# Kernel optimization log

Hardware: AMD Instinct MI355X
Metric: run time of the kernel (lower is better)

Reference implementation:

```python
import jax, jax.numpy as jnp
import numpy as np

EXTENT = 1.0  # kernel-point influence radius (init kwarg 'extent')
B, N, M, H, K, F, C = 4, 16384, 16384, 32, 15, 64, 64


def setup_inputs() -> dict:
    key = jax.random.key(0)
    ks = jax.random.split(key, 6)
    points = jax.random.uniform(ks[0], (B, N, 3), dtype=jnp.float32)
    features = jax.random.normal(ks[1], (B, N, F), dtype=jnp.float32)
    output_points = jax.random.uniform(ks[2], (B, M, 3), dtype=jnp.float32)
    neighbor_indices = jax.random.randint(ks[3], (B, M, H), 0, N)
    # kernel point dispositions inside a ball of radius 1.5*extent (load_kernels stand-in)
    k_points = jax.random.uniform(ks[4], (K, 3), minval=-1.0, maxval=1.0, dtype=jnp.float32) * (1.5 * EXTENT) / jnp.sqrt(3.0)
    k_values = jax.random.normal(ks[5], (K, F, C), dtype=jnp.float32) * 0.05
    return {
        'points': points, 'features': features, 'output_points': output_points,
        'k_points': k_points, 'k_values': k_values, 'neighbor_indices': neighbor_indices,
    }


def reference(points, features, output_points, k_points, k_values, neighbor_indices):
    b, m, h = neighbor_indices.shape
    idx = neighbor_indices.reshape(b, m * h, 1)
    # batched gather (tf.gather batch_dims=1)
    neigh_pts = jnp.take_along_axis(points, idx, axis=1).reshape(b, m, h, 3)
    neigh_feat = jnp.take_along_axis(features, idx, axis=1).reshape(b, m, h, -1)
    # relative coords to each output point, then to each kernel point
    rel = neigh_pts - output_points[:, :, None, :]                # [B,M,H,3]
    diff = rel[:, :, :, None, :] - k_points                       # [B,M,H,K,3]
    sq_d = jnp.sum(diff * diff, axis=-1)                          # [B,M,H,K]
    # linear influence
    w = jnp.maximum(1.0 - jnp.sqrt(sq_d) / EXTENT, 0.0)           # [B,M,H,K]
    # weight neighbor features per kernel point, then apply per-kernel linear map, sum over K
    wf = jnp.einsum('bmhk,bmhf->bmkf', w, neigh_feat)             # [B,M,K,F]
    out = jnp.einsum('bmkf,kfc->bmc', wf, k_values)               # [B,M,C]
    return out
```

## Files before the change

kernel.cpp:

```cpp
#include <hip/hip_runtime.h>

#define BATCH 4
#define NPTS 16384
#define MPTS 16384
#define NH 32
#define NK 15
#define NF 64
#define NC 64

typedef short short8 __attribute__((ext_vector_type(8)));
typedef float floatx4 __attribute__((ext_vector_type(4)));

__device__ __forceinline__ unsigned short f2bf(float x) {
    unsigned int u = __builtin_bit_cast(unsigned int, x);
    u = u + 0x7FFFu + ((u >> 16) & 1u);
    return (unsigned short)(u >> 16);
}

__device__ __forceinline__ unsigned pack_trunc(float lo, float hi) {
    return __builtin_amdgcn_perm(__builtin_bit_cast(unsigned, hi),
                                 __builtin_bit_cast(unsigned, lo), 0x07060302u);
}

__global__ void prep_kernel(const float* __restrict__ kv, const float* __restrict__ feat,
                            unsigned short* __restrict__ vp, unsigned short* __restrict__ featbf) {
    if (blockIdx.x < 32) {
        const int gid = blockIdx.x * 256 + threadIdx.x;
        const int lane = gid & 63;
        const int ct   = (gid >> 6) & 3;
        const int kk   = gid >> 8;
        const int c    = ct * 16 + (lane & 15);
        const int kap0 = kk * 32 + (lane >> 4) * 8;
        unsigned int o[4];
        #pragma unroll
        for (int jj = 0; jj < 4; jj++) {
            unsigned short lo, hi;
            {
                const int kap = kap0 + jj * 2;
                const int f = kap >> 4, k = kap & 15;
                lo = (k < NK) ? f2bf(kv[((size_t)(k * NF + f)) * NC + c]) : (unsigned short)0;
            }
            {
                const int kap = kap0 + jj * 2 + 1;
                const int f = kap >> 4, k = kap & 15;
                hi = (k < NK) ? f2bf(kv[((size_t)(k * NF + f)) * NC + c]) : (unsigned short)0;
            }
            o[jj] = (unsigned)lo | ((unsigned)hi << 16);
        }
        *(uint4*)(vp + (size_t)gid * 8) = make_uint4(o[0], o[1], o[2], o[3]);
    } else {
        const int gid = (blockIdx.x - 32) * 256 + threadIdx.x;
        const size_t base = (size_t)gid * 8;
        float4 a = *(const float4*)(feat + base);
        float4 b = *(const float4*)(feat + base + 4);
        uint4 o;
        o.x = (unsigned)f2bf(a.x) | ((unsigned)f2bf(a.y) << 16);
        o.y = (unsigned)f2bf(a.z) | ((unsigned)f2bf(a.w) << 16);
        o.z = (unsigned)f2bf(b.x) | ((unsigned)f2bf(b.y) << 16);
        o.w = (unsigned)f2bf(b.z) | ((unsigned)f2bf(b.w) << 16);
        *(uint4*)(featbf + base) = o;
    }
}

__global__ __launch_bounds__(256, 5) void kpconv_kernel(
    const float* __restrict__ points,
    const unsigned short* __restrict__ featbf,
    const float* __restrict__ outpts,
    const float* __restrict__ kpts,
    const unsigned short* __restrict__ vp,
    const int*   __restrict__ nbr,
    float* __restrict__ out)
{
    __shared__ __align__(16) unsigned short awf[16 * 512];
    __shared__ __align__(16) unsigned short feat_s[4 * 1160];
    __shared__ __align__(8) unsigned short idx_s[512];
    __shared__ float opt_s[48];
    __shared__ float kp_s[48];

    const int tid   = threadIdx.x;
    const int batch = blockIdx.x & 3;
    const int m0    = (blockIdx.x >> 2) << 4;

    if (tid < 48) kp_s[tid] = (tid < 45) ? kpts[tid] : 1e9f;
    if (tid >= 64 && tid < 112)
        opt_s[tid - 64] = outpts[(size_t)(batch * MPTS + m0) * 3 + (tid - 64)];
    {
        const size_t nb = (size_t)(batch * MPTS + m0) * NH;
        const int2 nn = *(const int2*)(nbr + nb + tid * 2);
        *(unsigned*)&idx_s[tid * 2] =
            (unsigned)(unsigned short)nn.x | ((unsigned)(unsigned short)nn.y << 16);
    }
    __syncthreads();

    const int g    = tid >> 6;
    const int lane = tid & 63;
    const int cl   = lane & 15;
    const int q    = lane >> 4;
    const int sa   = cl;
    const int sfc  = q;

    const unsigned short* fbase = featbf + (size_t)(batch * NPTS) * NF;

    uint4 praA, prbA, praB, prbB;
    {
        const int srow0 = (0 * 4 + g) * 32 + sa * 2;
        const int ida0 = idx_s[srow0], idb0 = idx_s[srow0 + 1];
        praA = *(const uint4*)(fbase + (size_t)ida0 * NF + sfc * 8);
        prbA = *(const uint4*)(fbase + (size_t)idb0 * NF + sfc * 8);
        const int srow1 = (1 * 4 + g) * 32 + sa * 2;
        const int ida1 = idx_s[srow1], idb1 = idx_s[srow1 + 1];
        praB = *(const uint4*)(fbase + (size_t)ida1 * NF + sfc * 8);
        prbB = *(const uint4*)(fbase + (size_t)idb1 * NF + sfc * 8);
    }

    float4* rel4 = (float4*)awf;
    #pragma unroll
    for (int rr = 0; rr < 2; rr++) {
        const int row = tid * 2 + rr;
        const int id  = idx_s[row];
        const int pm  = row >> 5;
        const float* pp = points + ((size_t)(batch * NPTS) + id) * 3;
        rel4[row + (row >> 3)] = make_float4(pp[0] - opt_s[pm * 3 + 0],
                                             pp[1] - opt_s[pm * 3 + 1],
                                             pp[2] - opt_s[pm * 3 + 2], 0.f);
    }
    __syncthreads();

    short8 af[4];
    {
        const float kx = kp_s[cl * 3 + 0];
        const float ky = kp_s[cl * 3 + 1];
        const float kz = kp_s[cl * 3 + 2];
        #pragma unroll
        for (int rp = 0; rp < 4; rp++) {
            const int p = rp * 4 + g;
            float wv[8];
            #pragma unroll
            for (int j = 0; j < 8; j++) {
                const float4 rr = rel4[36 * p + 9 * q + j];
                const float dx = rr.x - kx, dy = rr.y - ky, dz = rr.z - kz;
                const float d2 = dx * dx + dy * dy + dz * dz;
                wv[j] = fmaxf(1.f - __builtin_amdgcn_sqrtf(d2), 0.f);
            }
            uint4 ua;
            ua.x = pack_trunc(wv[0], wv[1]);
            ua.y = pack_trunc(wv[2], wv[3]);
            ua.z = pack_trunc(wv[4], wv[5]);
            ua.w = pack_trunc(wv[6], wv[7]);
            af[rp] = __builtin_bit_cast(short8, ua);
        }
    }
    __syncthreads();

    floatx4 acc0 = {0.f, 0.f, 0.f, 0.f};
    floatx4 acc1 = {0.f, 0.f, 0.f, 0.f};
    const unsigned short* vpg = vp + g * 512 + lane * 8;
    unsigned short* dp = &feat_s[g * 1160 + sfc * 288 + sa * 2];

    #pragma unroll
    for (int it = 0; it < 8; it++) {
        const int r  = it & 3;
        const int p  = r * 4 + g;

        *(unsigned*)(dp + 0 * 36) = __builtin_amdgcn_perm(prbA.x, praA.x, 0x05040100u);
        *(unsigned*)(dp + 1 * 36) = __builtin_amdgcn_perm(prbA.x, praA.x, 0x07060302u);
        *(unsigned*)(dp + 2 * 36) = __builtin_amdgcn_perm(prbA.y, praA.y, 0x05040100u);
        *(unsigned*)(dp + 3 * 36) = __builtin_amdgcn_perm(prbA.y, praA.y, 0x07060302u);
        *(unsigned*)(dp + 4 * 36) = __builtin_amdgcn_perm(prbA.z, praA.z, 0x05040100u);
        *(unsigned*)(dp + 5 * 36) = __builtin_amdgcn_perm(prbA.z, praA.z, 0x07060302u);
        *(unsigned*)(dp + 6 * 36) = __builtin_amdgcn_perm(prbA.w, praA.w, 0x05040100u);
        *(unsigned*)(dp + 7 * 36) = __builtin_amdgcn_perm(prbA.w, praA.w, 0x07060302u);

        praA = praB; prbA = prbB;
        if (it < 6) {
            const int nit = it + 2;
            const int nfh = nit >> 2, nr = nit & 3;
            const int srow = (nr * 4 + g) * 32 + sa * 2;
            const int id0 = idx_s[srow], id1 = idx_s[srow + 1];
            praB = *(const uint4*)(fbase + (size_t)id0 * NF + nfh * 32 + sfc * 8);
            prbB = *(const uint4*)(fbase + (size_t)id1 * NF + nfh * 32 + sfc * 8);
        }

        #pragma unroll
        for (int t = 0; t < 2; t++) {
            const uint4 ub = *(const uint4*)&feat_s[g * 1160 + (t * 16 + cl) * 36 + q * 8];
            floatx4 dd = {0.f, 0.f, 0.f, 0.f};
            dd = __builtin_amdgcn_mfma_f32_16x16x32_bf16(af[r], __builtin_bit_cast(short8, ub), dd, 0, 0, 0);
            const int kk    = 8 * t + (cl >> 1);
            const int q2    = (2 * cl + (q >> 1)) & 3;
            const int chunk = (p ^ kk) | (q2 << 4);
            unsigned* wp = (unsigned*)awf + kk * 256 + chunk * 4 + (q & 1) * 2;
            wp[0] = pack_trunc(dd[0], dd[1]);
            wp[1] = pack_trunc(dd[2], dd[3]);
        }

        if (it == 3) {
            __syncthreads();
            __builtin_amdgcn_s_setprio(1);
            #pragma unroll 4
            for (int kk = 0; kk < 16; kk++) {
                const int chunk = (cl ^ kk) | (lane & 48);
                const uint4 uA = *(const uint4*)&awf[kk * 512 + chunk * 8];
                const uint4 uB = *(const uint4*)(vpg + (size_t)kk * 2048);
                if (kk & 1)
                    acc1 = __builtin_amdgcn_mfma_f32_16x16x32_bf16(
                        __builtin_bit_cast(short8, uA), __builtin_bit_cast(short8, uB), acc1, 0, 0, 0);
                else
                    acc0 = __builtin_amdgcn_mfma_f32_16x16x32_bf16(
                        __builtin_bit_cast(short8, uA), __builtin_bit_cast(short8, uB), acc0, 0, 0, 0);
            }
            __builtin_amdgcn_s_setprio(0);
            __syncthreads();
        }
    }

    __syncthreads();
    __builtin_amdgcn_s_setprio(1);
    #pragma unroll 4
    for (int kk = 0; kk < 16; kk++) {
        const int chunk = (cl ^ kk) | (lane & 48);
        const uint4 uA = *(const uint4*)&awf[kk * 512 + chunk * 8];
        const uint4 uB = *(const uint4*)(vpg + (size_t)(16 + kk) * 2048);
        if (kk & 1)
            acc1 = __builtin_amdgcn_mfma_f32_16x16x32_bf16(
                __builtin_bit_cast(short8, uA), __builtin_bit_cast(short8, uB), acc1, 0, 0, 0);
        else
            acc0 = __builtin_amdgcn_mfma_f32_16x16x32_bf16(
                __builtin_bit_cast(short8, uA), __builtin_bit_cast(short8, uB), acc0, 0, 0, 0);
    }
    __builtin_amdgcn_s_setprio(0);

    __syncthreads();
    float* ob = (float*)awf;
    #pragma unroll
    for (int ri = 0; ri < 4; ri++)
        ob[(q * 4 + ri) * 68 + g * 16 + cl] = acc0[ri] + acc1[ri];
    __syncthreads();
    {
        const int row = tid >> 4;
        const int c4  = tid & 15;
        const floatx4 v = *(const floatx4*)&ob[row * 68 + c4 * 4];
        floatx4* dst = (floatx4*)&out[((size_t)(batch * MPTS + m0 + row)) * NC + c4 * 4];
        __builtin_nontemporal_store(v, dst);
    }
}

extern "C" void kernel_launch(void* const* d_in, const int* in_sizes, int n_in,
                              void* d_out, int out_size, void* d_ws, size_t ws_size,
                              hipStream_t stream) {
    const float* points   = (const float*)d_in[0];
    const float* features = (const float*)d_in[1];
    const float* outpts   = (const float*)d_in[2];
    const float* kpts     = (const float*)d_in[3];
    const float* kvals    = (const float*)d_in[4];
    const int*   nbr      = (const int*)d_in[5];
    float* out = (float*)d_out;

    unsigned short* vp     = (unsigned short*)d_ws;
    unsigned short* featbf = (unsigned short*)((char*)d_ws + 131072);

    prep_kernel<<<2080, 256, 0, stream>>>(kvals, features, vp, featbf);

    const int blocks = BATCH * (MPTS / 16);
    kpconv_kernel<<<blocks, 256, 0, stream>>>(points, featbf, outpts, kpts, vp, nbr, out);
}
```

Measured before the change: 137.2 us.

## Process 32 output points per 512-thread block, splitting kernel-point reduction across waves

Doubles the block tile from 16 to 32 output points with 8 waves. In the second GEMM each wave now handles two 16-row M tiles and half of the kernel-point range, so every B-fragment load of the packed kernel weights is reused across both tiles. Partial sums from the two kernel-point halves are combined through shared memory before the store. This cuts global weight traffic per output point and halves the block count, at the cost of doubled LDS per block, more accumulator registers and a tighter occupancy bound.

```diff
diff --git a/kernel.cpp b/kernel.cpp
--- a/kernel.cpp
+++ b/kernel.cpp
@@ -62,7 +62,7 @@
     }
 }
 
-__global__ __launch_bounds__(256, 5) void kpconv_kernel(
+__global__ __launch_bounds__(512, 6) void kpconv_kernel(
     const float* __restrict__ points,
     const unsigned short* __restrict__ featbf,
     const float* __restrict__ outpts,
@@ -71,18 +71,18 @@
     const int*   __restrict__ nbr,
     float* __restrict__ out)
 {
-    __shared__ __align__(16) unsigned short awf[16 * 512];
-    __shared__ __align__(16) unsigned short feat_s[4 * 1160];
-    __shared__ __align__(8) unsigned short idx_s[512];
-    __shared__ float opt_s[48];
+    __shared__ __align__(16) unsigned short awf[16 * 1024];
+    __shared__ __align__(16) unsigned short feat_s[8 * 1160];
+    __shared__ __align__(8) unsigned short idx_s[1024];
+    __shared__ float opt_s[96];
     __shared__ float kp_s[48];
 
     const int tid   = threadIdx.x;
     const int batch = blockIdx.x & 3;
-    const int m0    = (blockIdx.x >> 2) << 4;
+    const int m0    = (blockIdx.x >> 2) << 5;
 
     if (tid < 48) kp_s[tid] = (tid < 45) ? kpts[tid] : 1e9f;
-    if (tid >= 64 && tid < 112)
+    if (tid >= 64 && tid < 160)
         opt_s[tid - 64] = outpts[(size_t)(batch * MPTS + m0) * 3 + (tid - 64)];
     {
         const size_t nb = (size_t)(batch * MPTS + m0) * NH;
@@ -103,11 +103,11 @@
 
     uint4 praA, prbA, praB, prbB;
     {
-        const int srow0 = (0 * 4 + g) * 32 + sa * 2;
+        const int srow0 = (0 * 8 + g) * 32 + sa * 2;
         const int ida0 = idx_s[srow0], idb0 = idx_s[srow0 + 1];
         praA = *(const uint4*)(fbase + (size_t)ida0 * NF + sfc * 8);
         prbA = *(const uint4*)(fbase + (size_t)idb0 * NF + sfc * 8);
-        const int srow1 = (1 * 4 + g) * 32 + sa * 2;
+        const int srow1 = (1 * 8 + g) * 32 + sa * 2;
         const int ida1 = idx_s[srow1], idb1 = idx_s[srow1 + 1];
         praB = *(const uint4*)(fbase + (size_t)ida1 * NF + sfc * 8);
         prbB = *(const uint4*)(fbase + (size_t)idb1 * NF + sfc * 8);
@@ -133,7 +133,7 @@
         const float kz = kp_s[cl * 3 + 2];
         #pragma unroll
         for (int rp = 0; rp < 4; rp++) {
-            const int p = rp * 4 + g;
+            const int p = rp * 8 + g;
             float wv[8];
             #pragma unroll
             for (int j = 0; j < 8; j++) {
@@ -152,15 +152,21 @@
     }
     __syncthreads();
 
-    floatx4 acc0 = {0.f, 0.f, 0.f, 0.f};
-    floatx4 acc1 = {0.f, 0.f, 0.f, 0.f};
-    const unsigned short* vpg = vp + g * 512 + lane * 8;
+    floatx4 a00 = {0.f, 0.f, 0.f, 0.f};
+    floatx4 a01 = {0.f, 0.f, 0.f, 0.f};
+    floatx4 a10 = {0.f, 0.f, 0.f, 0.f};
+    floatx4 a11 = {0.f, 0.f, 0.f, 0.f};
+    const int ct  = g & 3;
+    const int kh8 = (g >> 2) * 8;
+    const unsigned short* vpg = vp + ct * 512 + lane * 8;
     unsigned short* dp = &feat_s[g * 1160 + sfc * 288 + sa * 2];
 
     #pragma unroll
     for (int it = 0; it < 8; it++) {
         const int r  = it & 3;
-        const int p  = r * 4 + g;
+        const int p  = r * 8 + g;
+        const int p4 = p & 15;
+        const int pu = p >> 4;
 
         *(unsigned*)(dp + 0 * 36) = __builtin_amdgcn_perm(prbA.x, praA.x, 0x05040100u);
         *(unsigned*)(dp + 1 * 36) = __builtin_amdgcn_perm(prbA.x, praA.x, 0x07060302u);
@@ -175,7 +181,7 @@
         if (it < 6) {
             const int nit = it + 2;
             const int nfh = nit >> 2, nr = nit & 3;
-            const int srow = (nr * 4 + g) * 32 + sa * 2;
+            const int srow = (nr * 8 + g) * 32 + sa * 2;
             const int id0 = idx_s[srow], id1 = idx_s[srow + 1];
             praB = *(const uint4*)(fbase + (size_t)id0 * NF + nfh * 32 + sfc * 8);
             prbB = *(const uint4*)(fbase + (size_t)id1 * NF + nfh * 32 + sfc * 8);
@@ -188,8 +194,8 @@
             dd = __builtin_amdgcn_mfma_f32_16x16x32_bf16(af[r], __builtin_bit_cast(short8, ub), dd, 0, 0, 0);
             const int kk    = 8 * t + (cl >> 1);
             const int q2    = (2 * cl + (q >> 1)) & 3;
-            const int chunk = (p ^ kk) | (q2 << 4);
-            unsigned* wp = (unsigned*)awf + kk * 256 + chunk * 4 + (q & 1) * 2;
+            const int chunk = (p4 ^ kk) | (q2 << 4) | (pu << 6);
+            unsigned* wp = (unsigned*)awf + kk * 512 + chunk * 4 + (q & 1) * 2;
             wp[0] = pack_trunc(dd[0], dd[1]);
             wp[1] = pack_trunc(dd[2], dd[3]);
         }
@@ -198,16 +204,23 @@
             __syncthreads();
             __builtin_amdgcn_s_setprio(1);
             #pragma unroll 4
-            for (int kk = 0; kk < 16; kk++) {
-                const int chunk = (cl ^ kk) | (lane & 48);
-                const uint4 uA = *(const uint4*)&awf[kk * 512 + chunk * 8];
-                const uint4 uB = *(const uint4*)(vpg + (size_t)kk * 2048);
-                if (kk & 1)
-                    acc1 = __builtin_amdgcn_mfma_f32_16x16x32_bf16(
-                        __builtin_bit_cast(short8, uA), __builtin_bit_cast(short8, uB), acc1, 0, 0, 0);
-                else
-                    acc0 = __builtin_amdgcn_mfma_f32_16x16x32_bf16(
-                        __builtin_bit_cast(short8, uA), __builtin_bit_cast(short8, uB), acc0, 0, 0, 0);
+            for (int kkl = 0; kkl < 8; kkl++) {
+                const int kka = kh8 + kkl;
+                const uint4 uB = *(const uint4*)(vpg + (size_t)kka * 2048);
+                const int ch = (cl ^ kka) | (q << 4);
+                const uint4 uA0 = *(const uint4*)&awf[kka * 1024 + ch * 8];
+                const uint4 uA1 = *(const uint4*)&awf[kka * 1024 + (ch | 64) * 8];
+                if (kkl & 1) {
+                    a01 = __builtin_amdgcn_mfma_f32_16x16x32_bf16(
+                        __builtin_bit_cast(short8, uA0), __builtin_bit_cast(short8, uB), a01, 0, 0, 0);
+                    a11 = __builtin_amdgcn_mfma_f32_16x16x32_bf16(
+                        __builtin_bit_cast(short8, uA1), __builtin_bit_cast(short8, uB), a11, 0, 0, 0);
+                } else {
+                    a00 = __builtin_amdgcn_mfma_f32_16x16x32_bf16(
+                        __builtin_bit_cast(short8, uA0), __builtin_bit_cast(short8, uB), a00, 0, 0, 0);
+                    a10 = __builtin_amdgcn_mfma_f32_16x16x32_bf16(
+                        __builtin_bit_cast(short8, uA1), __builtin_bit_cast(short8, uB), a10, 0, 0, 0);
+                }
             }
             __builtin_amdgcn_s_setprio(0);
             __syncthreads();
@@ -217,29 +230,41 @@
     __syncthreads();
     __builtin_amdgcn_s_setprio(1);
     #pragma unroll 4
-    for (int kk = 0; kk < 16; kk++) {
-        const int chunk = (cl ^ kk) | (lane & 48);
-        const uint4 uA = *(const uint4*)&awf[kk * 512 + chunk * 8];
-        const uint4 uB = *(const uint4*)(vpg + (size_t)(16 + kk) * 2048);
-        if (kk & 1)
-            acc1 = __builtin_amdgcn_mfma_f32_16x16x32_bf16(
-                __builtin_bit_cast(short8, uA), __builtin_bit_cast(short8, uB), acc1, 0, 0, 0);
-        else
-            acc0 = __builtin_amdgcn_mfma_f32_16x16x32_bf16(
-                __builtin_bit_cast(short8, uA), __builtin_bit_cast(short8, uB), acc0, 0, 0, 0);
+    for (int kkl = 0; kkl < 8; kkl++) {
+        const int kka = kh8 + kkl;
+        const uint4 uB = *(const uint4*)(vpg + (size_t)(16 + kka) * 2048);
+        const int ch = (cl ^ kka) | (q << 4);
+        const uint4 uA0 = *(const uint4*)&awf[kka * 1024 + ch * 8];
+        const uint4 uA1 = *(const uint4*)&awf[kka * 1024 + (ch | 64) * 8];
+        if (kkl & 1) {
+            a01 = __builtin_amdgcn_mfma_f32_16x16x32_bf16(
+                __builtin_bit_cast(short8, uA0), __builtin_bit_cast(short8, uB), a01, 0, 0, 0);
+            a11 = __builtin_amdgcn_mfma_f32_16x16x32_bf16(
+                __builtin_bit_cast(short8, uA1), __builtin_bit_cast(short8, uB), a11, 0, 0, 0);
+        } else {
+            a00 = __builtin_amdgcn_mfma_f32_16x16x32_bf16(
+                __builtin_bit_cast(short8, uA0), __builtin_bit_cast(short8, uB), a00, 0, 0, 0);
+            a10 = __builtin_amdgcn_mfma_f32_16x16x32_bf16(
+                __builtin_bit_cast(short8, uA1), __builtin_bit_cast(short8, uB), a10, 0, 0, 0);
+        }
     }
     __builtin_amdgcn_s_setprio(0);
 
     __syncthreads();
     float* ob = (float*)awf;
+    const int kh = g >> 2;
     #pragma unroll
-    for (int ri = 0; ri < 4; ri++)
-        ob[(q * 4 + ri) * 68 + g * 16 + cl] = acc0[ri] + acc1[ri];
+    for (int ri = 0; ri < 4; ri++) {
+        ob[(kh * 32 +      q * 4 + ri) * 68 + ct * 16 + cl] = a00[ri] + a01[ri];
+        ob[(kh * 32 + 16 + q * 4 + ri) * 68 + ct * 16 + cl] = a10[ri] + a11[ri];
+    }
     __syncthreads();
     {
         const int row = tid >> 4;
         const int c4  = tid & 15;
-        const floatx4 v = *(const floatx4*)&ob[row * 68 + c4 * 4];
+        const floatx4 v0 = *(const floatx4*)&ob[row * 68 + c4 * 4];
+        const floatx4 v1 = *(const floatx4*)&ob[(32 + row) * 68 + c4 * 4];
+        const floatx4 v = v0 + v1;
         floatx4* dst = (floatx4*)&out[((size_t)(batch * MPTS + m0 + row)) * NC + c4 * 4];
         __builtin_nontemporal_store(v, dst);
     }
@@ -261,6 +286,6 @@
 
     prep_kernel<<<2080, 256, 0, stream>>>(kvals, features, vp, featbf);
 
-    const int blocks = BATCH * (MPTS / 16);
-    kpconv_kernel<<<blocks, 256, 0, stream>>>(points, featbf, outpts, kpts, vp, nbr, out);
-}
+    const int blocks = BATCH * (MPTS / 32);
+    kpconv_kernel<<<blocks, 512, 0, stream>>>(points, featbf, outpts, kpts, vp, nbr, out);
+}
```

Measured after the change: 147.8 us. +7.7%, slower.

## Double the weighted-feature LDS buffer and run one fused second-stage MFMA pass

Applied to the files above, without the earlier changes.

The shared weighted-feature buffer now holds both feature halves (32 slices instead of 16). The mid-loop stage-2 MFMA pass at it==3 and its two barriers are removed, and a single 32-step contraction runs after the loop. This cuts barrier stalls and gives the MFMA loop a longer run. In exchange it doubles that LDS allocation, and launch bounds drop from 5 to 4 blocks per CU, which reduces occupancy.

```diff
diff --git a/kernel.cpp b/kernel.cpp
--- a/kernel.cpp
+++ b/kernel.cpp
@@ -62,7 +62,7 @@
     }
 }
 
-__global__ __launch_bounds__(256, 5) void kpconv_kernel(
+__global__ __launch_bounds__(256, 4) void kpconv_kernel(
     const float* __restrict__ points,
     const unsigned short* __restrict__ featbf,
     const float* __restrict__ outpts,
@@ -71,7 +71,7 @@
     const int*   __restrict__ nbr,
     float* __restrict__ out)
 {
-    __shared__ __align__(16) unsigned short awf[16 * 512];
+    __shared__ __align__(16) unsigned short awf[32 * 512];
     __shared__ __align__(16) unsigned short feat_s[4 * 1160];
     __shared__ __align__(8) unsigned short idx_s[512];
     __shared__ float opt_s[48];
@@ -152,8 +152,6 @@
     }
     __syncthreads();
 
-    floatx4 acc0 = {0.f, 0.f, 0.f, 0.f};
-    floatx4 acc1 = {0.f, 0.f, 0.f, 0.f};
     const unsigned short* vpg = vp + g * 512 + lane * 8;
     unsigned short* dp = &feat_s[g * 1160 + sfc * 288 + sa * 2];
 
@@ -161,6 +159,7 @@
     for (int it = 0; it < 8; it++) {
         const int r  = it & 3;
         const int p  = r * 4 + g;
+        const int fh = it >> 2;
 
         *(unsigned*)(dp + 0 * 36) = __builtin_amdgcn_perm(prbA.x, praA.x, 0x05040100u);
         *(unsigned*)(dp + 1 * 36) = __builtin_amdgcn_perm(prbA.x, praA.x, 0x07060302u);
@@ -187,41 +186,26 @@
             floatx4 dd = {0.f, 0.f, 0.f, 0.f};
             dd = __builtin_amdgcn_mfma_f32_16x16x32_bf16(af[r], __builtin_bit_cast(short8, ub), dd, 0, 0, 0);
             const int kk    = 8 * t + (cl >> 1);
+            const int kka   = fh * 16 + kk;
             const int q2    = (2 * cl + (q >> 1)) & 3;
             const int chunk = (p ^ kk) | (q2 << 4);
-            unsigned* wp = (unsigned*)awf + kk * 256 + chunk * 4 + (q & 1) * 2;
+            unsigned* wp = (unsigned*)awf + kka * 256 + chunk * 4 + (q & 1) * 2;
             wp[0] = pack_trunc(dd[0], dd[1]);
             wp[1] = pack_trunc(dd[2], dd[3]);
         }
-
-        if (it == 3) {
-            __syncthreads();
-            __builtin_amdgcn_s_setprio(1);
-            #pragma unroll 4
-            for (int kk = 0; kk < 16; kk++) {
-                const int chunk = (cl ^ kk) | (lane & 48);
-                const uint4 uA = *(const uint4*)&awf[kk * 512 + chunk * 8];
-                const uint4 uB = *(const uint4*)(vpg + (size_t)kk * 2048);
-                if (kk & 1)
-                    acc1 = __builtin_amdgcn_mfma_f32_16x16x32_bf16(
-                        __builtin_bit_cast(short8, uA), __builtin_bit_cast(short8, uB), acc1, 0, 0, 0);
-                else
-                    acc0 = __builtin_amdgcn_mfma_f32_16x16x32_bf16(
-                        __builtin_bit_cast(short8, uA), __builtin_bit_cast(short8, uB), acc0, 0, 0, 0);
-            }
-            __builtin_amdgcn_s_setprio(0);
-            __syncthreads();
-        }
-    }
-
-    __syncthreads();
+    }
+
+    __syncthreads();
+
+    floatx4 acc0 = {0.f, 0.f, 0.f, 0.f};
+    floatx4 acc1 = {0.f, 0.f, 0.f, 0.f};
     __builtin_amdgcn_s_setprio(1);
-    #pragma unroll 4
-    for (int kk = 0; kk < 16; kk++) {
-        const int chunk = (cl ^ kk) | (lane & 48);
-        const uint4 uA = *(const uint4*)&awf[kk * 512 + chunk * 8];
-        const uint4 uB = *(const uint4*)(vpg + (size_t)(16 + kk) * 2048);
-        if (kk & 1)
+    #pragma unroll 8
+    for (int kka = 0; kka < 32; kka++) {
+        const int chunk = (cl ^ (kka & 15)) | (lane & 48);
+        const uint4 uA = *(const uint4*)&awf[kka * 512 + chunk * 8];
+        const uint4 uB = *(const uint4*)(vpg + (size_t)kka * 2048);
+        if (kka & 1)
             acc1 = __builtin_amdgcn_mfma_f32_16x16x32_bf16(
                 __builtin_bit_cast(short8, uA), __builtin_bit_cast(short8, uB), acc1, 0, 0, 0);
         else
```

New measurement: 141.2 us. 2.9% more time.
